# Performance work log

Hardware: AMD Instinct MI355X
Metric: run time of the kernel (lower is better)

Reference implementation:

```python
import jax, jax.numpy as jnp
import numpy as np

N_NODES = 10000
N_EDGES = 640000
NF = 128
HID = 128
NORM_FACTOR = 100.0


def setup_inputs() -> dict:
    key = jax.random.key(0)
    ks = jax.random.split(key, 8)
    s = lambda fan_in: 1.0 / np.sqrt(fan_in)
    return {
        "h": jax.random.normal(ks[0], (N_NODES, NF), dtype=jnp.float32),
        "edge_index": jax.random.randint(ks[1], (2, N_EDGES), 0, N_NODES, dtype=jnp.int64),
        "ew1": jax.random.normal(ks[2], (2 * NF, HID), dtype=jnp.float32) * s(2 * NF),
        "eb1": jnp.zeros((HID,), dtype=jnp.float32),
        "ew2": jax.random.normal(ks[3], (HID, HID), dtype=jnp.float32) * s(HID),
        "eb2": jnp.zeros((HID,), dtype=jnp.float32),
        "nw1": jax.random.normal(ks[4], (HID + NF, HID), dtype=jnp.float32) * s(HID + NF),
        "nb1": jnp.zeros((HID,), dtype=jnp.float32),
        "nw2": jax.random.normal(ks[5], (HID, NF), dtype=jnp.float32) * s(HID),
        "nb2": jnp.zeros((NF,), dtype=jnp.float32),
    }


def reference(h, edge_index, ew1, eb1, ew2, eb2, nw1, nb1, nw2, nb2):
    row, col = edge_index[0], edge_index[1]
    # edge model: gather endpoints, concat, 2-layer SiLU MLP -> mij [E, HID]
    x = jnp.concatenate([h[row], h[col]], axis=1)          # [E, 2*NF]
    mij = jax.nn.silu(x @ ew1 + eb1)
    mij = jax.nn.silu(mij @ ew2 + eb2)                     # [E, HID]
    # aggregation: scatter-add messages to source nodes, 'sum' normalization
    agg = jax.ops.segment_sum(mij, row, num_segments=h.shape[0]) / NORM_FACTOR
    # node model: residual MLP update
    a = jnp.concatenate([h, agg], axis=1)                  # [V, NF+HID]
    out = h + (jax.nn.silu(a @ nw1 + nb1) @ nw2 + nb2)     # [V, NF]
    return out, mij
```

## Files before the change

kernel.cpp:

```cpp
#include <hip/hip_runtime.h>

typedef __attribute__((ext_vector_type(8))) short short8;
typedef __attribute__((ext_vector_type(4))) float f32x4;
typedef unsigned short ushort_t;
typedef unsigned int uint_t;

#define MFMA16(a, b, c) __builtin_amdgcn_mfma_f32_16x16x32_bf16((a), (b), (c), 0, 0, 0)

constexpr int V = 10000;
constexpr int E = 640000;
constexpr int NF = 128;
constexpr int XS_STRIDE = 264;
constexpr int YS_STRIDE = 136;

__device__ __forceinline__ ushort_t f2b(float f) {
    uint_t u = __float_as_uint(f);
    u += 0x7FFFu + ((u >> 16) & 1u);
    return (ushort_t)(u >> 16);
}

__device__ __forceinline__ float silu(float x) {
    return x / (1.0f + __expf(-x));
}

__global__ void cvt_f32_bf16(const float* __restrict__ src, ushort_t* __restrict__ dst, int n) {
    int i = blockIdx.x * blockDim.x + threadIdx.x;
    if (i < n) dst[i] = f2b(src[i]);
}

__global__ __launch_bounds__(256, 2) void edge_kernel(
    const ushort_t* __restrict__ hb, const int* __restrict__ eidx,
    const ushort_t* __restrict__ w1, const float* __restrict__ eb1,
    const ushort_t* __restrict__ w2, const float* __restrict__ eb2,
    float* __restrict__ mij, float* __restrict__ agg) {
    __shared__ __align__(16) ushort_t xs[64 * XS_STRIDE];
    __shared__ __align__(16) ushort_t ys[64 * YS_STRIDE];
    __shared__ int ridx[64];

    const int tid = threadIdx.x;
    const int wave = tid >> 6;
    const int lane = tid & 63;
    const int quad = lane >> 4;
    const int ln = lane & 15;
    const int ncol0 = wave * 32;

    short8 b1f[8][2];
    short8 b2f[4][2];
#pragma unroll
    for (int kk = 0; kk < 8; kk++)
#pragma unroll
        for (int t = 0; t < 2; t++) {
            short8 f;
#pragma unroll
            for (int j = 0; j < 8; j++)
                f[j] = ((const short*)w1)[(kk * 32 + quad * 8 + j) * 128 + ncol0 + t * 16 + ln];
            b1f[kk][t] = f;
        }
#pragma unroll
    for (int kk = 0; kk < 4; kk++)
#pragma unroll
        for (int t = 0; t < 2; t++) {
            short8 f;
#pragma unroll
            for (int j = 0; j < 8; j++)
                f[j] = ((const short*)w2)[(kk * 32 + quad * 8 + j) * 128 + ncol0 + t * 16 + ln];
            b2f[kk][t] = f;
        }
    const float bv1[2] = {eb1[ncol0 + ln], eb1[ncol0 + 16 + ln]};
    const float bv2[2] = {eb2[ncol0 + ln], eb2[ncol0 + 16 + ln]};

    for (int tile = blockIdx.x; tile < E / 64; tile += gridDim.x) {
        const int e0 = tile * 64;
        {
            const int e = tid >> 2, seg = tid & 3;
            const int r = eidx[e0 + e];
            const int c = eidx[E + e0 + e];
            if (seg == 0) ridx[e] = r;
            const int node = (seg < 2) ? r : c;
            const uint4* src = (const uint4*)(hb + node * 128 + (seg & 1) * 64);
            uint4* dst = (uint4*)(xs + e * XS_STRIDE + seg * 64);
#pragma unroll
            for (int u = 0; u < 8; u++) dst[u] = src[u];
        }
        __syncthreads();

        f32x4 acc[4][2];
#pragma unroll
        for (int mt = 0; mt < 4; mt++)
#pragma unroll
            for (int t = 0; t < 2; t++) acc[mt][t] = f32x4{bv1[t], bv1[t], bv1[t], bv1[t]};
#pragma unroll
        for (int kk = 0; kk < 8; kk++) {
#pragma unroll
            for (int mt = 0; mt < 4; mt++) {
                short8 a = *(const short8*)(xs + (mt * 16 + ln) * XS_STRIDE + kk * 32 + quad * 8);
                acc[mt][0] = MFMA16(a, b1f[kk][0], acc[mt][0]);
                acc[mt][1] = MFMA16(a, b1f[kk][1], acc[mt][1]);
            }
        }
#pragma unroll
        for (int mt = 0; mt < 4; mt++)
#pragma unroll
            for (int t = 0; t < 2; t++) {
#pragma unroll
                for (int r = 0; r < 4; r++) {
                    float s = silu(acc[mt][t][r]);
                    ys[(mt * 16 + quad * 4 + r) * YS_STRIDE + ncol0 + t * 16 + ln] = f2b(s);
                }
            }
        __syncthreads();

        f32x4 acc2[4][2];
#pragma unroll
        for (int mt = 0; mt < 4; mt++)
#pragma unroll
            for (int t = 0; t < 2; t++) acc2[mt][t] = f32x4{bv2[t], bv2[t], bv2[t], bv2[t]};
#pragma unroll
        for (int kk = 0; kk < 4; kk++) {
#pragma unroll
            for (int mt = 0; mt < 4; mt++) {
                short8 a = *(const short8*)(ys + (mt * 16 + ln) * YS_STRIDE + kk * 32 + quad * 8);
                acc2[mt][0] = MFMA16(a, b2f[kk][0], acc2[mt][0]);
                acc2[mt][1] = MFMA16(a, b2f[kk][1], acc2[mt][1]);
            }
        }

#pragma unroll
        for (int mt = 0; mt < 4; mt++) {
#pragma unroll
            for (int r = 0; r < 4; r++) {
                const int row = mt * 16 + quad * 4 + r;
                const int nsrc = ridx[row];
#pragma unroll
                for (int t = 0; t < 2; t++) {
                    float s = silu(acc2[mt][t][r]);
                    const int col = ncol0 + t * 16 + ln;
                    mij[(size_t)(e0 + row) * 128 + col] = s;
                    unsafeAtomicAdd(&agg[nsrc * 128 + col], s);
                }
            }
        }
        __syncthreads();
    }
}

__global__ __launch_bounds__(256, 2) void node_kernel(
    const ushort_t* __restrict__ hb, const float* __restrict__ h32,
    const float* __restrict__ agg,
    const ushort_t* __restrict__ w1, const float* __restrict__ nb1,
    const ushort_t* __restrict__ w2, const float* __restrict__ nb2,
    float* __restrict__ out) {
    __shared__ __align__(16) ushort_t xs[64 * XS_STRIDE];
    __shared__ __align__(16) ushort_t ys[64 * YS_STRIDE];

    const int tid = threadIdx.x;
    const int wave = tid >> 6;
    const int lane = tid & 63;
    const int quad = lane >> 4;
    const int ln = lane & 15;
    const int ncol0 = wave * 32;
    const int i0 = blockIdx.x * 64;

    short8 b1f[8][2];
    short8 b2f[4][2];
#pragma unroll
    for (int kk = 0; kk < 8; kk++)
#pragma unroll
        for (int t = 0; t < 2; t++) {
            short8 f;
#pragma unroll
            for (int j = 0; j < 8; j++)
                f[j] = ((const short*)w1)[(kk * 32 + quad * 8 + j) * 128 + ncol0 + t * 16 + ln];
            b1f[kk][t] = f;
        }
#pragma unroll
    for (int kk = 0; kk < 4; kk++)
#pragma unroll
        for (int t = 0; t < 2; t++) {
            short8 f;
#pragma unroll
            for (int j = 0; j < 8; j++)
                f[j] = ((const short*)w2)[(kk * 32 + quad * 8 + j) * 128 + ncol0 + t * 16 + ln];
            b2f[kk][t] = f;
        }
    const float bv1[2] = {nb1[ncol0 + ln], nb1[ncol0 + 16 + ln]};
    const float bv2[2] = {nb2[ncol0 + ln], nb2[ncol0 + 16 + ln]};

    {
        const int e = tid >> 2, seg = tid & 3;
        const int node = i0 + e;
        if (node < V) {
            if (seg < 2) {
                const uint4* src = (const uint4*)(hb + node * 128 + seg * 64);
                uint4* dst = (uint4*)(xs + e * XS_STRIDE + seg * 64);
#pragma unroll
                for (int u = 0; u < 8; u++) dst[u] = src[u];
            } else {
                const float4* src = (const float4*)(agg + node * 128 + (seg & 1) * 64);
                ushort4* dst = (ushort4*)(xs + e * XS_STRIDE + seg * 64);
#pragma unroll
                for (int u = 0; u < 16; u++) {
                    float4 v = src[u];
                    ushort4 o;
                    o.x = f2b(v.x * 0.01f);
                    o.y = f2b(v.y * 0.01f);
                    o.z = f2b(v.z * 0.01f);
                    o.w = f2b(v.w * 0.01f);
                    dst[u] = o;
                }
            }
        } else {
            uint4 z{0, 0, 0, 0};
            uint4* dst = (uint4*)(xs + e * XS_STRIDE + seg * 64);
#pragma unroll
            for (int u = 0; u < 8; u++) dst[u] = z;
        }
    }
    __syncthreads();

    f32x4 acc[4][2];
#pragma unroll
    for (int mt = 0; mt < 4; mt++)
#pragma unroll
        for (int t = 0; t < 2; t++) acc[mt][t] = f32x4{bv1[t], bv1[t], bv1[t], bv1[t]};
#pragma unroll
    for (int kk = 0; kk < 8; kk++) {
#pragma unroll
        for (int mt = 0; mt < 4; mt++) {
            short8 a = *(const short8*)(xs + (mt * 16 + ln) * XS_STRIDE + kk * 32 + quad * 8);
            acc[mt][0] = MFMA16(a, b1f[kk][0], acc[mt][0]);
            acc[mt][1] = MFMA16(a, b1f[kk][1], acc[mt][1]);
        }
    }
#pragma unroll
    for (int mt = 0; mt < 4; mt++)
#pragma unroll
        for (int t = 0; t < 2; t++) {
#pragma unroll
            for (int r = 0; r < 4; r++) {
                float s = silu(acc[mt][t][r]);
                ys[(mt * 16 + quad * 4 + r) * YS_STRIDE + ncol0 + t * 16 + ln] = f2b(s);
            }
        }
    __syncthreads();

    f32x4 acc2[4][2];
#pragma unroll
    for (int mt = 0; mt < 4; mt++)
#pragma unroll
        for (int t = 0; t < 2; t++) acc2[mt][t] = f32x4{bv2[t], bv2[t], bv2[t], bv2[t]};
#pragma unroll
    for (int kk = 0; kk < 4; kk++) {
#pragma unroll
        for (int mt = 0; mt < 4; mt++) {
            short8 a = *(const short8*)(ys + (mt * 16 + ln) * YS_STRIDE + kk * 32 + quad * 8);
            acc2[mt][0] = MFMA16(a, b2f[kk][0], acc2[mt][0]);
            acc2[mt][1] = MFMA16(a, b2f[kk][1], acc2[mt][1]);
        }
    }
#pragma unroll
    for (int mt = 0; mt < 4; mt++) {
#pragma unroll
        for (int r = 0; r < 4; r++) {
            const int row = mt * 16 + quad * 4 + r;
            const int node = i0 + row;
            if (node < V) {
#pragma unroll
                for (int t = 0; t < 2; t++) {
                    const int col = ncol0 + t * 16 + ln;
                    out[(size_t)node * 128 + col] = h32[(size_t)node * 128 + col] + acc2[mt][t][r];
                }
            }
        }
    }
}

extern "C" void kernel_launch(void* const* d_in, const int* in_sizes, int n_in,
                              void* d_out, int out_size, void* d_ws, size_t ws_size,
                              hipStream_t stream) {
    const float* h = (const float*)d_in[0];
    const int* eidx = (const int*)d_in[1];
    const float* ew1 = (const float*)d_in[2];
    const float* eb1 = (const float*)d_in[3];
    const float* ew2 = (const float*)d_in[4];
    const float* eb2 = (const float*)d_in[5];
    const float* nw1 = (const float*)d_in[6];
    const float* nb1 = (const float*)d_in[7];
    const float* nw2 = (const float*)d_in[8];
    const float* nb2 = (const float*)d_in[9];

    float* out = (float*)d_out;
    float* mij = (float*)d_out + (size_t)V * 128;

    uint8_t* ws = (uint8_t*)d_ws;
    ushort_t* hb = (ushort_t*)(ws);
    ushort_t* w1b = (ushort_t*)(ws + 2560000);
    ushort_t* w2b = (ushort_t*)(ws + 2560000 + 65536);
    ushort_t* nw1b = (ushort_t*)(ws + 2560000 + 98304);
    ushort_t* nw2b = (ushort_t*)(ws + 2560000 + 163840);
    float* agg = (float*)(ws + 2560000 + 196608);

    hipMemsetAsync(agg, 0, (size_t)V * 128 * sizeof(float), stream);

    cvt_f32_bf16<<<(V * 128 + 255) / 256, 256, 0, stream>>>(h, hb, V * 128);
    cvt_f32_bf16<<<128, 256, 0, stream>>>(ew1, w1b, 256 * 128);
    cvt_f32_bf16<<<64, 256, 0, stream>>>(ew2, w2b, 128 * 128);
    cvt_f32_bf16<<<128, 256, 0, stream>>>(nw1, nw1b, 256 * 128);
    cvt_f32_bf16<<<64, 256, 0, stream>>>(nw2, nw2b, 128 * 128);

    edge_kernel<<<2048, 256, 0, stream>>>(hb, eidx, w1b, eb1, w2b, eb2, mij, agg);
    node_kernel<<<(V + 63) / 64, 256, 0, stream>>>(hb, h, agg, nw1b, nb1, nw2b, nb2, out);
}
```

Before: 599.0 us.

## Prefetch next edge tile gather, swizzle LDS, transpose weights, fuse prep kernels

The edge kernel now loads the next tile's endpoint rows and indices into registers while the current tile runs its first GEMM, then writes them to LDS after the first barrier, with double-buffered row indices. LDS padding is replaced by an XOR swizzle. Weights are pre-transposed so B fragments become single 16-byte loads. The five conversion kernels and the memset are merged into one prep kernel, and the grid is set to 2000 so tiles divide evenly. The risks are higher register pressure from the prefetch buffers and reduced occupancy.

```diff
diff --git a/kernel.cpp b/kernel.cpp
--- a/kernel.cpp
+++ b/kernel.cpp
@@ -9,9 +9,6 @@
 
 constexpr int V = 10000;
 constexpr int E = 640000;
-constexpr int NF = 128;
-constexpr int XS_STRIDE = 264;
-constexpr int YS_STRIDE = 136;
 
 __device__ __forceinline__ ushort_t f2b(float f) {
     uint_t u = __float_as_uint(f);
@@ -23,9 +20,37 @@
     return x / (1.0f + __expf(-x));
 }
 
-__global__ void cvt_f32_bf16(const float* __restrict__ src, ushort_t* __restrict__ dst, int n) {
+__device__ __forceinline__ uint_t cvt_pk_bf16(float lo, float hi) {
+    uint_t r;
+    asm("v_cvt_pk_bf16_f32 %0, %1, %2" : "=v"(r) : "v"(lo), "v"(hi));
+    return r;
+}
+
+__device__ __forceinline__ void wg_barrier_lds() {
+    asm volatile("s_waitcnt lgkmcnt(0)" ::: "memory");
+    __builtin_amdgcn_s_barrier();
+    asm volatile("" ::: "memory");
+}
+
+__global__ void prep(const float* __restrict__ h,
+                     const float* __restrict__ ew1, const float* __restrict__ ew2,
+                     const float* __restrict__ nw1, const float* __restrict__ nw2,
+                     ushort_t* __restrict__ hb,
+                     ushort_t* __restrict__ w1T, ushort_t* __restrict__ w2T,
+                     ushort_t* __restrict__ nw1T, ushort_t* __restrict__ nw2T,
+                     float* __restrict__ agg) {
     int i = blockIdx.x * blockDim.x + threadIdx.x;
-    if (i < n) dst[i] = f2b(src[i]);
+    if (i < V * 128) { hb[i] = f2b(h[i]); return; }
+    i -= V * 128;
+    if (i < V * 128) { agg[i] = 0.0f; return; }
+    i -= V * 128;
+    if (i < 256 * 128) { int k = i >> 7, c = i & 127; w1T[c * 256 + k] = f2b(ew1[i]); return; }
+    i -= 256 * 128;
+    if (i < 128 * 128) { int k = i >> 7, c = i & 127; w2T[c * 128 + k] = f2b(ew2[i]); return; }
+    i -= 128 * 128;
+    if (i < 256 * 128) { int k = i >> 7, c = i & 127; nw1T[c * 256 + k] = f2b(nw1[i]); return; }
+    i -= 256 * 128;
+    if (i < 128 * 128) { int k = i >> 7, c = i & 127; nw2T[c * 128 + k] = f2b(nw2[i]); }
 }
 
 __global__ __launch_bounds__(256, 2) void edge_kernel(
@@ -33,9 +58,9 @@
     const ushort_t* __restrict__ w1, const float* __restrict__ eb1,
     const ushort_t* __restrict__ w2, const float* __restrict__ eb2,
     float* __restrict__ mij, float* __restrict__ agg) {
-    __shared__ __align__(16) ushort_t xs[64 * XS_STRIDE];
-    __shared__ __align__(16) ushort_t ys[64 * YS_STRIDE];
-    __shared__ int ridx[64];
+    __shared__ __align__(16) ushort_t xs[64 * 256];
+    __shared__ __align__(16) ushort_t ys[64 * 128];
+    __shared__ int ridx[2][64];
 
     const int tid = threadIdx.x;
     const int wave = tid >> 6;
@@ -49,40 +74,49 @@
 #pragma unroll
     for (int kk = 0; kk < 8; kk++)
 #pragma unroll
-        for (int t = 0; t < 2; t++) {
-            short8 f;
-#pragma unroll
-            for (int j = 0; j < 8; j++)
-                f[j] = ((const short*)w1)[(kk * 32 + quad * 8 + j) * 128 + ncol0 + t * 16 + ln];
-            b1f[kk][t] = f;
-        }
+        for (int t = 0; t < 2; t++)
+            b1f[kk][t] = *(const short8*)(w1 + (ncol0 + t * 16 + ln) * 256 + kk * 32 + quad * 8);
 #pragma unroll
     for (int kk = 0; kk < 4; kk++)
 #pragma unroll
-        for (int t = 0; t < 2; t++) {
-            short8 f;
-#pragma unroll
-            for (int j = 0; j < 8; j++)
-                f[j] = ((const short*)w2)[(kk * 32 + quad * 8 + j) * 128 + ncol0 + t * 16 + ln];
-            b2f[kk][t] = f;
-        }
+        for (int t = 0; t < 2; t++)
+            b2f[kk][t] = *(const short8*)(w2 + (ncol0 + t * 16 + ln) * 128 + kk * 32 + quad * 8);
     const float bv1[2] = {eb1[ncol0 + ln], eb1[ncol0 + 16 + ln]};
     const float bv2[2] = {eb2[ncol0 + ln], eb2[ncol0 + 16 + ln]};
 
-    for (int tile = blockIdx.x; tile < E / 64; tile += gridDim.x) {
+    const int NT = E / 64;
+    const int e = lane;
+    const int seg = wave;
+    char* const xrow = (char*)xs + e * 512;
+    const int xswz = (e & 7) << 4;
+
+    int tile = blockIdx.x;
+
+    {
+        const int r = eidx[tile * 64 + e];
+        const int c = eidx[E + tile * 64 + e];
+        if (seg == 0) ridx[0][e] = r;
+        const int node = (seg < 2) ? r : c;
+        const uint4* src = (const uint4*)(hb + node * 128 + (seg & 1) * 64);
+#pragma unroll
+        for (int u = 0; u < 8; u++)
+            *(uint4*)(xrow + ((seg * 128 + u * 16) ^ xswz)) = src[u];
+    }
+    wg_barrier_lds();
+
+    int p = 0;
+    for (; tile < NT; tile += gridDim.x) {
         const int e0 = tile * 64;
-        {
-            const int e = tid >> 2, seg = tid & 3;
-            const int r = eidx[e0 + e];
-            const int c = eidx[E + e0 + e];
-            if (seg == 0) ridx[e] = r;
-            const int node = (seg < 2) ? r : c;
-            const uint4* src = (const uint4*)(hb + node * 128 + (seg & 1) * 64);
-            uint4* dst = (uint4*)(xs + e * XS_STRIDE + seg * 64);
-#pragma unroll
-            for (int u = 0; u < 8; u++) dst[u] = src[u];
-        }
-        __syncthreads();
+        int tn = tile + gridDim.x;
+        if (tn >= NT) tn = tile;
+
+        const int rn = eidx[tn * 64 + e];
+        const int cn = eidx[E + tn * 64 + e];
+        const int noden = (seg < 2) ? rn : cn;
+        const uint4* srcn = (const uint4*)(hb + noden * 128 + (seg & 1) * 64);
+        uint4 st[8];
+#pragma unroll
+        for (int u = 0; u < 8; u++) st[u] = srcn[u];
 
         f32x4 acc[4][2];
 #pragma unroll
@@ -90,25 +124,33 @@
 #pragma unroll
             for (int t = 0; t < 2; t++) acc[mt][t] = f32x4{bv1[t], bv1[t], bv1[t], bv1[t]};
 #pragma unroll
-        for (int kk = 0; kk < 8; kk++) {
+        for (int kk = 0; kk < 8; kk++)
 #pragma unroll
             for (int mt = 0; mt < 4; mt++) {
-                short8 a = *(const short8*)(xs + (mt * 16 + ln) * XS_STRIDE + kk * 32 + quad * 8);
+                const int row = mt * 16 + ln;
+                short8 a = *(const short8*)((char*)xs + row * 512 +
+                                            ((kk * 64 + quad * 16) ^ ((ln & 7) << 4)));
                 acc[mt][0] = MFMA16(a, b1f[kk][0], acc[mt][0]);
                 acc[mt][1] = MFMA16(a, b1f[kk][1], acc[mt][1]);
             }
-        }
 #pragma unroll
         for (int mt = 0; mt < 4; mt++)
 #pragma unroll
-            for (int t = 0; t < 2; t++) {
-#pragma unroll
-                for (int r = 0; r < 4; r++) {
-                    float s = silu(acc[mt][t][r]);
-                    ys[(mt * 16 + quad * 4 + r) * YS_STRIDE + ncol0 + t * 16 + ln] = f2b(s);
-                }
-            }
-        __syncthreads();
+            for (int r4 = 0; r4 < 4; r4++) {
+                const int row = mt * 16 + quad * 4 + r4;
+                const uint_t pk = cvt_pk_bf16(silu(acc[mt][0][r4]), silu(acc[mt][1][r4]));
+                char* yrow = (char*)ys + row * 256;
+                const int ysw = (row & 7) << 4;
+                const int cb = 2 * (ncol0 + ln);
+                *(ushort_t*)(yrow + (cb ^ ysw)) = (ushort_t)pk;
+                *(ushort_t*)(yrow + ((cb + 32) ^ ysw)) = (ushort_t)(pk >> 16);
+            }
+        wg_barrier_lds();
+
+        if (seg == 0) ridx[p ^ 1][e] = rn;
+#pragma unroll
+        for (int u = 0; u < 8; u++)
+            *(uint4*)(xrow + ((seg * 128 + u * 16) ^ xswz)) = st[u];
 
         f32x4 acc2[4][2];
 #pragma unroll
@@ -116,31 +158,32 @@
 #pragma unroll
             for (int t = 0; t < 2; t++) acc2[mt][t] = f32x4{bv2[t], bv2[t], bv2[t], bv2[t]};
 #pragma unroll
-        for (int kk = 0; kk < 4; kk++) {
+        for (int kk = 0; kk < 4; kk++)
 #pragma unroll
             for (int mt = 0; mt < 4; mt++) {
-                short8 a = *(const short8*)(ys + (mt * 16 + ln) * YS_STRIDE + kk * 32 + quad * 8);
+                const int row = mt * 16 + ln;
+                short8 a = *(const short8*)((char*)ys + row * 256 +
+                                            ((kk * 64 + quad * 16) ^ ((ln & 7) << 4)));
                 acc2[mt][0] = MFMA16(a, b2f[kk][0], acc2[mt][0]);
                 acc2[mt][1] = MFMA16(a, b2f[kk][1], acc2[mt][1]);
             }
-        }
-
-#pragma unroll
-        for (int mt = 0; mt < 4; mt++) {
-#pragma unroll
-            for (int r = 0; r < 4; r++) {
-                const int row = mt * 16 + quad * 4 + r;
-                const int nsrc = ridx[row];
+
+#pragma unroll
+        for (int mt = 0; mt < 4; mt++)
+#pragma unroll
+            for (int r4 = 0; r4 < 4; r4++) {
+                const int row = mt * 16 + quad * 4 + r4;
+                const int nsrc = ridx[p][row];
 #pragma unroll
                 for (int t = 0; t < 2; t++) {
-                    float s = silu(acc2[mt][t][r]);
+                    const float s = silu(acc2[mt][t][r4]);
                     const int col = ncol0 + t * 16 + ln;
                     mij[(size_t)(e0 + row) * 128 + col] = s;
                     unsafeAtomicAdd(&agg[nsrc * 128 + col], s);
                 }
             }
-        }
-        __syncthreads();
+        wg_barrier_lds();
+        p ^= 1;
     }
 }
 
@@ -150,8 +193,8 @@
     const ushort_t* __restrict__ w1, const float* __restrict__ nb1,
     const ushort_t* __restrict__ w2, const float* __restrict__ nb2,
     float* __restrict__ out) {
-    __shared__ __align__(16) ushort_t xs[64 * XS_STRIDE];
-    __shared__ __align__(16) ushort_t ys[64 * YS_STRIDE];
+    __shared__ __align__(16) ushort_t xs[64 * 256];
+    __shared__ __align__(16) ushort_t ys[64 * 128];
 
     const int tid = threadIdx.x;
     const int wave = tid >> 6;
@@ -166,55 +209,45 @@
 #pragma unroll
     for (int kk = 0; kk < 8; kk++)
 #pragma unroll
-        for (int t = 0; t < 2; t++) {
-            short8 f;
-#pragma unroll
-            for (int j = 0; j < 8; j++)
-                f[j] = ((const short*)w1)[(kk * 32 + quad * 8 + j) * 128 + ncol0 + t * 16 + ln];
-            b1f[kk][t] = f;
-        }
+        for (int t = 0; t < 2; t++)
+            b1f[kk][t] = *(const short8*)(w1 + (ncol0 + t * 16 + ln) * 256 + kk * 32 + quad * 8);
 #pragma unroll
     for (int kk = 0; kk < 4; kk++)
 #pragma unroll
-        for (int t = 0; t < 2; t++) {
-            short8 f;
-#pragma unroll
-            for (int j = 0; j < 8; j++)
-                f[j] = ((const short*)w2)[(kk * 32 + quad * 8 + j) * 128 + ncol0 + t * 16 + ln];
-            b2f[kk][t] = f;
-        }
+        for (int t = 0; t < 2; t++)
+            b2f[kk][t] = *(const short8*)(w2 + (ncol0 + t * 16 + ln) * 128 + kk * 32 + quad * 8);
     const float bv1[2] = {nb1[ncol0 + ln], nb1[ncol0 + 16 + ln]};
     const float bv2[2] = {nb2[ncol0 + ln], nb2[ncol0 + 16 + ln]};
 
-    {
-        const int e = tid >> 2, seg = tid & 3;
-        const int node = i0 + e;
-        if (node < V) {
-            if (seg < 2) {
-                const uint4* src = (const uint4*)(hb + node * 128 + seg * 64);
-                uint4* dst = (uint4*)(xs + e * XS_STRIDE + seg * 64);
-#pragma unroll
-                for (int u = 0; u < 8; u++) dst[u] = src[u];
-            } else {
-                const float4* src = (const float4*)(agg + node * 128 + (seg & 1) * 64);
-                ushort4* dst = (ushort4*)(xs + e * XS_STRIDE + seg * 64);
-#pragma unroll
-                for (int u = 0; u < 16; u++) {
-                    float4 v = src[u];
-                    ushort4 o;
-                    o.x = f2b(v.x * 0.01f);
-                    o.y = f2b(v.y * 0.01f);
-                    o.z = f2b(v.z * 0.01f);
-                    o.w = f2b(v.w * 0.01f);
-                    dst[u] = o;
-                }
-            }
+    const int e = lane, seg = wave;
+    char* const xrow = (char*)xs + e * 512;
+    const int xswz = (e & 7) << 4;
+    const int node = i0 + e;
+
+    if (node < V) {
+        if (seg < 2) {
+            const uint4* src = (const uint4*)(hb + node * 128 + seg * 64);
+#pragma unroll
+            for (int u = 0; u < 8; u++)
+                *(uint4*)(xrow + ((seg * 128 + u * 16) ^ xswz)) = src[u];
         } else {
-            uint4 z{0, 0, 0, 0};
-            uint4* dst = (uint4*)(xs + e * XS_STRIDE + seg * 64);
-#pragma unroll
-            for (int u = 0; u < 8; u++) dst[u] = z;
-        }
+            const float4* src = (const float4*)(agg + node * 128 + (seg & 1) * 64);
+#pragma unroll
+            for (int u = 0; u < 8; u++) {
+                float4 a = src[2 * u], b = src[2 * u + 1];
+                uint4 v;
+                v.x = cvt_pk_bf16(a.x * 0.01f, a.y * 0.01f);
+                v.y = cvt_pk_bf16(a.z * 0.01f, a.w * 0.01f);
+                v.z = cvt_pk_bf16(b.x * 0.01f, b.y * 0.01f);
+                v.w = cvt_pk_bf16(b.z * 0.01f, b.w * 0.01f);
+                *(uint4*)(xrow + ((seg * 128 + u * 16) ^ xswz)) = v;
+            }
+        }
+    } else {
+        const uint4 z{0, 0, 0, 0};
+#pragma unroll
+        for (int u = 0; u < 8; u++)
+            *(uint4*)(xrow + ((seg * 128 + u * 16) ^ xswz)) = z;
     }
     __syncthreads();
 
@@ -224,23 +257,26 @@
 #pragma unroll
         for (int t = 0; t < 2; t++) acc[mt][t] = f32x4{bv1[t], bv1[t], bv1[t], bv1[t]};
 #pragma unroll
-    for (int kk = 0; kk < 8; kk++) {
+    for (int kk = 0; kk < 8; kk++)
 #pragma unroll
         for (int mt = 0; mt < 4; mt++) {
-            short8 a = *(const short8*)(xs + (mt * 16 + ln) * XS_STRIDE + kk * 32 + quad * 8);
+            const int row = mt * 16 + ln;
+            short8 a = *(const short8*)((char*)xs + row * 512 +
+                                        ((kk * 64 + quad * 16) ^ ((ln & 7) << 4)));
             acc[mt][0] = MFMA16(a, b1f[kk][0], acc[mt][0]);
             acc[mt][1] = MFMA16(a, b1f[kk][1], acc[mt][1]);
         }
-    }
 #pragma unroll
     for (int mt = 0; mt < 4; mt++)
 #pragma unroll
-        for (int t = 0; t < 2; t++) {
-#pragma unroll
-            for (int r = 0; r < 4; r++) {
-                float s = silu(acc[mt][t][r]);
-                ys[(mt * 16 + quad * 4 + r) * YS_STRIDE + ncol0 + t * 16 + ln] = f2b(s);
-            }
+        for (int r4 = 0; r4 < 4; r4++) {
+            const int row = mt * 16 + quad * 4 + r4;
+            const uint_t pk = cvt_pk_bf16(silu(acc[mt][0][r4]), silu(acc[mt][1][r4]));
+            char* yrow = (char*)ys + row * 256;
+            const int ysw = (row & 7) << 4;
+            const int cb = 2 * (ncol0 + ln);
+            *(ushort_t*)(yrow + (cb ^ ysw)) = (ushort_t)pk;
+            *(ushort_t*)(yrow + ((cb + 32) ^ ysw)) = (ushort_t)(pk >> 16);
         }
     __syncthreads();
 
@@ -250,29 +286,29 @@
 #pragma unroll
         for (int t = 0; t < 2; t++) acc2[mt][t] = f32x4{bv2[t], bv2[t], bv2[t], bv2[t]};
 #pragma unroll
-    for (int kk = 0; kk < 4; kk++) {
+    for (int kk = 0; kk < 4; kk++)
 #pragma unroll
         for (int mt = 0; mt < 4; mt++) {
-            short8 a = *(const short8*)(ys + (mt * 16 + ln) * YS_STRIDE + kk * 32 + quad * 8);
+            const int row = mt * 16 + ln;
+            short8 a = *(const short8*)((char*)ys + row * 256 +
+                                        ((kk * 64 + quad * 16) ^ ((ln & 7) << 4)));
             acc2[mt][0] = MFMA16(a, b2f[kk][0], acc2[mt][0]);
             acc2[mt][1] = MFMA16(a, b2f[kk][1], acc2[mt][1]);
         }
-    }
-#pragma unroll
-    for (int mt = 0; mt < 4; mt++) {
-#pragma unroll
-        for (int r = 0; r < 4; r++) {
-            const int row = mt * 16 + quad * 4 + r;
-            const int node = i0 + row;
-            if (node < V) {
+#pragma unroll
+    for (int mt = 0; mt < 4; mt++)
+#pragma unroll
+        for (int r4 = 0; r4 < 4; r4++) {
+            const int row = mt * 16 + quad * 4 + r4;
+            const int nd = i0 + row;
+            if (nd < V) {
 #pragma unroll
                 for (int t = 0; t < 2; t++) {
                     const int col = ncol0 + t * 16 + ln;
-                    out[(size_t)node * 128 + col] = h32[(size_t)node * 128 + col] + acc2[mt][t][r];
+                    out[(size_t)nd * 128 + col] = h32[(size_t)nd * 128 + col] + acc2[mt][t][r4];
                 }
             }
         }
-    }
 }
 
 extern "C" void kernel_launch(void* const* d_in, const int* in_sizes, int n_in,
@@ -300,14 +336,10 @@
     ushort_t* nw2b = (ushort_t*)(ws + 2560000 + 163840);
     float* agg = (float*)(ws + 2560000 + 196608);
 
-    hipMemsetAsync(agg, 0, (size_t)V * 128 * sizeof(float), stream);
-
-    cvt_f32_bf16<<<(V * 128 + 255) / 256, 256, 0, stream>>>(h, hb, V * 128);
-    cvt_f32_bf16<<<128, 256, 0, stream>>>(ew1, w1b, 256 * 128);
-    cvt_f32_bf16<<<64, 256, 0, stream>>>(ew2, w2b, 128 * 128);
-    cvt_f32_bf16<<<128, 256, 0, stream>>>(nw1, nw1b, 256 * 128);
-    cvt_f32_bf16<<<64, 256, 0, stream>>>(nw2, nw2b, 128 * 128);
-
-    edge_kernel<<<2048, 256, 0, stream>>>(hb, eidx, w1b, eb1, w2b, eb2, mij, agg);
+    constexpr int PREP_N = V * 128 + V * 128 + 256 * 128 + 128 * 128 + 256 * 128 + 128 * 128;
+    prep<<<(PREP_N + 255) / 256, 256, 0, stream>>>(h, ew1, ew2, nw1, nw2,
+                                                   hb, w1b, w2b, nw1b, nw2b, agg);
+
+    edge_kernel<<<2000, 256, 0, stream>>>(hb, eidx, w1b, eb1, w2b, eb2, mij, agg);
     node_kernel<<<(V + 63) / 64, 256, 0, stream>>>(hb, h, agg, nw1b, nb1, nw2b, nb2, out);
 }
```

After: 604.5 us. Within noise of the previous version (+0.9%).
